# Performance work log

Measured on AMD Instinct MI355X. Metric: run time of the kernel, lower is better.

Reference implementation:

```python
import jax, jax.numpy as jnp
import numpy as np

N_NODES = 10000
N_EDGES = 320000
IN_FEATS = 500
CONV_DIMS = [500, 256, 256]
FC_DIMS = [256, 128, 40]
BN_EPS = 1e-5


def setup_inputs() -> dict:
    key = jax.random.key(0)
    ks = jax.random.split(key, 16)
    inp = {
        "x": jax.random.normal(ks[0], (N_NODES, IN_FEATS), dtype=jnp.float32),
        "edge_index": jax.random.randint(ks[1], (2, N_EDGES), 0, N_NODES, dtype=jnp.int64),
    }
    # conv layer params: Linear W [in,out], b [out]; BatchNorm gamma/beta [out]
    ki = 2
    for li in range(len(CONV_DIMS) - 1):
        d_in, d_out = CONV_DIMS[li], CONV_DIMS[li + 1]
        s = 1.0 / np.sqrt(d_in)
        inp[f"conv_W{li}"] = jax.random.uniform(ks[ki], (d_in, d_out), jnp.float32, -s, s); ki += 1
        inp[f"conv_b{li}"] = jax.random.uniform(ks[ki], (d_out,), jnp.float32, -s, s); ki += 1
        inp[f"bn_g{li}"] = jnp.ones((d_out,), jnp.float32)
        inp[f"bn_b{li}"] = jnp.zeros((d_out,), jnp.float32)
    for li in range(len(FC_DIMS) - 1):
        d_in, d_out = FC_DIMS[li], FC_DIMS[li + 1]
        s = 1.0 / np.sqrt(d_in)
        inp[f"fc_W{li}"] = jax.random.uniform(ks[ki], (d_in, d_out), jnp.float32, -s, s); ki += 1
        inp[f"fc_b{li}"] = jax.random.uniform(ks[ki], (d_out,), jnp.float32, -s, s); ki += 1
    return inp


def _degree(edge_index, n, dtype):
    # Faithful to: A = eye(N); A[i,j] = 1 per edge (set semantics dedupes repeats).
    A = jnp.eye(n, dtype=dtype).at[edge_index[0], edge_index[1]].set(1.0)
    return A.sum(axis=1)  # deg_i = rowsum of A


def _batchnorm(h, g, b):
    # training-mode BatchNorm1d: batch stats, biased variance
    mean = h.mean(axis=0)
    var = h.var(axis=0)
    return (h - mean) * jax.lax.rsqrt(var + BN_EPS) * g + b


def reference(x, edge_index, conv_W0, conv_b0, bn_g0, bn_b0,
              conv_W1, conv_b1, bn_g1, bn_b1,
              fc_W0, fc_b0, fc_W1, fc_b1):
    n = x.shape[0]
    deg = _degree(edge_index, n, x.dtype)
    # D = sqrt(diag(deg)) is a diagonal matrix, so elementwise D*A*D = diag(deg);
    # mm(D*A*D, x) == deg[:, None] * x (exactly the original math).
    h = x
    for W, b, g, beta in ((conv_W0, conv_b0, bn_g0, bn_b0),
                          (conv_W1, conv_b1, bn_g1, bn_b1)):
        h = (deg[:, None] * h) @ W + b
        h = jax.nn.relu(h)
        h = _batchnorm(h, g, beta)
        # dropout: identity at inference
    for W, b in ((fc_W0, fc_b0), (fc_W1, fc_b1)):
        h = jax.nn.relu(h @ W + b)  # original appends ReLU after every fc, incl. last
    return h
```

## Files before the change

kernel.cpp:

```cpp
#include <hip/hip_runtime.h>

#define NN 10000
#define NE 320000
#define MP 10112
#define BN_EPS 1e-5f

#define NRANGE 64
#define BROWS 160
#define NBUCK 128
#define HBITS 5120
#define HWORDS 160
#define SUBCAP 128
#define EPB   5000

typedef __attribute__((ext_vector_type(8))) short short8;
typedef __attribute__((ext_vector_type(4))) float f32x4;
typedef unsigned short u16;

__device__ __forceinline__ void split1(float v, u16& h, u16& l) {
    unsigned int u = __float_as_uint(v);
    h = (u16)(u >> 16);
    float hf = __uint_as_float(u & 0xFFFF0000u);
    l = (u16)(__float_as_uint(v - hf) >> 16);
}

__device__ __forceinline__ void gll16(const void* g, void* l) {
    __builtin_amdgcn_global_load_lds(
        (const __attribute__((address_space(1))) unsigned int*)g,
        (__attribute__((address_space(3))) unsigned int*)l, 16, 0, 0);
}

__device__ void splitW_dev(const float* __restrict__ W, int K, int N, int Kp, int Np,
                           u16* __restrict__ Wt, int bx, int by, char* smem) {
    float (*tile)[65] = (float(*)[65])smem;
    int t = threadIdx.x;
    int bk = bx * 64, bn = by * 64;
    #pragma unroll
    for (int p = 0; p < 4; ++p) {
        int kk = (t >> 4) + p * 16;
        int nc = (t & 15) * 4;
        int k = bk + kk;
        float4 v = {0.f, 0.f, 0.f, 0.f};
        if (k < K && bn + nc + 3 < N)
            v = *(const float4*)&W[(size_t)k * N + bn + nc];
        tile[kk][nc] = v.x; tile[kk][nc + 1] = v.y;
        tile[kk][nc + 2] = v.z; tile[kk][nc + 3] = v.w;
    }
    __syncthreads();
    int nn = t >> 2;
    int kk0 = (t & 3) * 16;
    u16 hs[16], ls[16];
    #pragma unroll
    for (int j = 0; j < 16; ++j) split1(tile[kk0 + j][nn], hs[j], ls[j]);
    size_t ob = (size_t)(bn + nn) * Kp + bk + kk0;
    size_t lo = (size_t)Np * Kp;
    *(short8*)&Wt[ob] = *(short8*)hs;
    *(short8*)&Wt[ob + 8] = *(short8*)&hs[8];
    *(short8*)&Wt[lo + ob] = *(short8*)ls;
    *(short8*)&Wt[lo + ob + 8] = *(short8*)&ls[8];
}

__global__ __launch_bounds__(256)
void scatter_prep(const int* __restrict__ ei,
                  unsigned* __restrict__ bucketArr, unsigned* __restrict__ cnts,
                  float* __restrict__ stats, float* __restrict__ zpad,
                  const float* __restrict__ W0, const float* __restrict__ fW1,
                  u16* __restrict__ W0t, u16* __restrict__ fW1t) {
    __shared__ char smem[16704];
    __shared__ unsigned cnt[NBUCK];
    int b = blockIdx.x;
    int t = threadIdx.x;
    if (b < 64) {
        if (t < NBUCK) cnt[t] = 0;
        __syncthreads();
        int base = b * EPB;
        #pragma unroll
        for (int k = 0; k < 20; ++k) {
            int el = t + k * 256;
            if (el < EPB) {
                int e = base + el;
                unsigned i = (unsigned)ei[e], j = (unsigned)ei[NE + e];
                unsigned bk = (i / BROWS) * 2 + (j >= HBITS ? 1u : 0u);
                unsigned key = (i << 14) | j;
                unsigned pos = atomicAdd(&cnt[bk], 1u);
                if (pos < SUBCAP)
                    bucketArr[((size_t)bk << 13) + ((unsigned)b << 7) + pos] = key;
            }
        }
        __syncthreads();
        if (t < NBUCK) cnts[(t << 6) + b] = min(cnt[t], (unsigned)SUBCAP);
    } else if (b < 96) {
        int idx = b - 64;
        splitW_dev(W0, 500, 256, 512, 256, W0t, idx & 7, idx >> 3, smem);
    } else {
        int base = (b - 96) * 512;
        stats[base + t] = 0.f;
        stats[base + 256 + t] = 0.f;
        if (b == 96 && t < 64) zpad[t] = 0.f;
        splitW_dev(fW1, 128, 40, 128, 64, fW1t, b - 96, 0, smem);
    }
}

__global__ __launch_bounds__(256)
void bucket_degree(const unsigned* __restrict__ bucketArr,
                   const unsigned* __restrict__ cnts,
                   float* __restrict__ degh) {
    __shared__ unsigned lbm[BROWS * HWORDS];
    int b = blockIdx.x, t = threadIdx.x;
    int rr = b >> 1, h = b & 1;
    int row0 = rr * BROWS;
    {
        uint4* z = (uint4*)lbm;
        #pragma unroll
        for (int i = 0; i < 25; ++i) z[t + i * 256] = (uint4){0u, 0u, 0u, 0u};
    }
    __syncthreads();
    for (int r = t; r < BROWS; r += 256) {
        int i = row0 + r;
        if (i < NN && ((i >= HBITS) == (h == 1))) {
            int jj = i - h * HBITS;
            atomicOr(&lbm[r * HWORDS + (jj >> 5)], 1u << (jj & 31));
        }
    }
    {
        int sb = t >> 2, kl = t & 3;
        unsigned n = cnts[(b << 6) + sb];
        const unsigned* keys = bucketArr + ((size_t)b << 13) + ((unsigned)sb << 7);
        for (unsigned k = kl; k < n; k += 4) {
            unsigned key = keys[k];
            unsigned i = key >> 14, j = key & 0x3FFFu;
            unsigned r = i - row0;
            unsigned jj = j - h * HBITS;
            atomicOr(&lbm[r * HWORDS + (jj >> 5)], 1u << (jj & 31));
        }
    }
    __syncthreads();
    #pragma unroll
    for (int pass = 0; pass < 3; ++pass) {
        int r = pass * 64 + (t >> 2), wl = t & 3;
        if (r >= BROWS) break;
        int i = row0 + r;
        int c = 0;
        const uint4* rp = (const uint4*)&lbm[r * HWORDS + wl * 40];
        #pragma unroll
        for (int m = 0; m < 10; ++m) {
            uint4 v = rp[m];
            c += __popc(v.x) + __popc(v.y) + __popc(v.z) + __popc(v.w);
        }
        c += __shfl_down(c, 1, 4);
        c += __shfl_down(c, 2, 4);
        if (wl == 0 && i < MP) degh[h * MP + i] = (float)c;
    }
}

__global__ __launch_bounds__(256, 3)
void conv0_gemm(const float* __restrict__ x, const float* __restrict__ zpad,
                const u16* __restrict__ Bhi, const u16* __restrict__ Blo,
                const float* __restrict__ degh, const float* __restrict__ bias,
                float* __restrict__ stats,
                u16* __restrict__ Ohi, u16* __restrict__ Olo) {
    __shared__ char smem[49152];
    __shared__ float sdeg[64];
    const int Kp = 512, M = NN, No = 256;
    const int b = blockIdx.x;
    const int xcd = b & 7, g = b >> 3;
    const int bx = g & 3, by = (g >> 2) * 8 + xcd;
    if (by >= 158) return;
    const int t = threadIdx.x;
    const int lane = t & 63;
    const int w = t >> 6;
    const int q = lane >> 4;
    const int l16 = lane & 15;
    const int m7 = l16 & 7;
    const int row0 = by * 64;
    const int col0 = bx * 64;

    const u16* srcs[4];
    unsigned dstoff[4];
    #pragma unroll
    for (int i = 0; i < 4; ++i) {
        int j = w + (i & 1) * 4;
        int plane = i >> 1;
        int r = j * 8 + (lane >> 3);
        int c = (lane & 7) ^ (r & 7);
        srcs[i] = (plane ? Blo : Bhi) + (size_t)(col0 + r) * Kp + c * 8;
        dstoff[i] = 16384 + plane * 8192 + j * 1024;
    }

    int xrow[4];
    int xcol[4];
    unsigned xdst[4];
    #pragma unroll
    for (int i = 0; i < 4; ++i) {
        int slab = w * 4 + i;
        int row = slab * 4 + (lane >> 4);
        int cl = (lane & 15) ^ (row & 15);
        xrow[i] = row0 + row;
        xcol[i] = cl * 4;
        xdst[i] = 32768 + slab * 1024;
    }

    #pragma unroll
    for (int i = 0; i < 4; ++i) gll16(srcs[i], smem + dstoff[i]);
    #pragma unroll
    for (int i = 0; i < 4; ++i) {
        int col = xcol[i];
        const float* s = (xrow[i] < NN && col < 500)
                       ? x + (size_t)xrow[i] * 500 + col : zpad;
        gll16(s, smem + xdst[i]);
    }

    if (t < 64) sdeg[t] = degh[row0 + t] + degh[MP + row0 + t];

    __syncthreads();

    const int rn = t & 63;
    const int c4 = t >> 6;
// ... 66 lines not shown
            if (k0 + 128 < Kp) {
                #pragma unroll
                for (int i = 0; i < 4; ++i) {
                    int col = k0 + 128 + xcol[i];
                    const float* s = (xrow[i] < NN && col < 500)
                                   ? x + (size_t)xrow[i] * 500 + col : zpad;
                    gll16(s, smem + xdst[i]);
                }
            }
        }
        #pragma unroll
        for (int kc = 0; kc < 2; ++kc)
            #pragma unroll
            for (int s = 0; s < 4; ++s) {
                acc[s] = __builtin_amdgcn_mfma_f32_16x16x32_bf16(al[kc], bh[kc][s], acc[s], 0, 0, 0);
                acc[s] = __builtin_amdgcn_mfma_f32_16x16x32_bf16(ah[kc], bl[kc][s], acc[s], 0, 0, 0);
                acc[s] = __builtin_amdgcn_mfma_f32_16x16x32_bf16(ah[kc], bh[kc][s], acc[s], 0, 0, 0);
            }
    }

    int growb = row0 + w * 16 + q * 4;
    float dgv[4];
    #pragma unroll
    for (int r = 0; r < 4; ++r) {
        int grow = growb + r;
        dgv[r] = (grow < M) ? sdeg[grow - row0] : 0.f;
    }
    #pragma unroll
    for (int s = 0; s < 4; ++s) {
        int gc = col0 + s * 16 + l16;
        float bia = bias[gc];
        float s_sum = 0.f, ss_sum = 0.f;
        #pragma unroll
        for (int r = 0; r < 4; ++r) {
            int grow = growb + r;
            bool real = grow < M;
            float v = fmaxf(fmaf(dgv[r], acc[s][r], bia), 0.f);
            if (!real) v = 0.f;
            s_sum += v; ss_sum += v * v;
            float vo = v * dgv[r];
            u16 h, l; split1(vo, h, l);
            Ohi[(size_t)grow * No + gc] = h;
            Olo[(size_t)grow * No + gc] = l;
        }
        s_sum  += __shfl_xor(s_sum, 16);  s_sum  += __shfl_xor(s_sum, 32);
        ss_sum += __shfl_xor(ss_sum, 16); ss_sum += __shfl_xor(ss_sum, 32);
        if (lane < 16) {
            atomicAdd(&stats[gc], s_sum);
            atomicAdd(&stats[256 + gc], ss_sum);
        }
    }
}

__global__ __launch_bounds__(256, 4)
void conv1_fold(const u16* __restrict__ Ahi, const u16* __restrict__ Alo,
                const float* __restrict__ W1, const float* __restrict__ stats0,
                const float* __restrict__ g0, const float* __restrict__ bb0,
                const float* __restrict__ b1, const float* __restrict__ degh,
                float* __restrict__ stats1, u16* __restrict__ Ohi, u16* __restrict__ Olo) {
    __shared__ char smem[32768];
    __shared__ float scl[256], sh[256], cred[256], cvec[64];
    const int Kp = 256, M = NN, No = 256;
    const int b = blockIdx.x;
    const int xcd = b & 7, g = b >> 3;
    const int bx = g & 3, by = (g >> 2) * 8 + xcd;
    if (by >= 158) return;
    const int t = threadIdx.x;
    const int lane = t & 63;
    const int w = t >> 6;
    const int q = lane >> 4;
    const int l16 = lane & 15;
    const int m7 = l16 & 7;
    const int row0 = by * 64;
    const int col0 = bx * 64;

    const u16* srcs[4];
    unsigned dstoff[4];
    #pragma unroll
    for (int i = 0; i < 4; ++i) {
        int gi = w + i * 4;
        int plane = gi >> 3, j = gi & 7;
        int r = j * 8 + (lane >> 3);
        int c = (lane & 7) ^ (r & 7);
        srcs[i] = (plane ? Alo : Ahi) + (size_t)(row0 + r) * Kp + c * 8;
        dstoff[i] = plane * 8192 + j * 1024;
    }
    #pragma unroll
    for (int i = 0; i < 4; ++i) { gll16(srcs[i], smem + dstoff[i]); srcs[i] += 64; }

    {
        float mean = stats0[t] * (1.f / NN);
        float var = stats0[256 + t] * (1.f / NN) - mean * mean;
        float s = g0[t] * rsqrtf(var + BN_EPS);
        scl[t] = s;
        sh[t] = bb0[t] - mean * s;
    }
    __syncthreads();
    {
        float s = 0.f;
        int n = col0 + (t & 63);
        #pragma unroll 8
        for (int k = (t >> 6); k < 256; k += 4)
            s += sh[k] * W1[(size_t)k * 256 + n];
        cred[t] = s;
        __syncthreads();
        if (t < 64) cvec[t] = cred[t] + cred[t + 64] + cred[t + 128] + cred[t + 192];
    }
    const int bn = t & 63;
    const int kb = (t >> 6) * 16;
    const int ch0 = (t >> 6) * 2;
    float vals[16];
    {
        const float* wp = W1 + (size_t)kb * 256 + col0 + bn;
        #pragma unroll
        for (int i = 0; i < 16; ++i) vals[i] = wp[(size_t)i * 256] * scl[kb + i];
    }
// ... 29 lines not shown
            }
        }
        __syncthreads();
        if (k0 + 64 < Kp) {
            #pragma unroll
            for (int i = 0; i < 4; ++i) { gll16(srcs[i], smem + dstoff[i]); srcs[i] += 64; }
            const float* wp = W1 + (size_t)(k0 + 64 + kb) * 256 + col0 + bn;
            #pragma unroll
            for (int i = 0; i < 16; ++i) vals[i] = wp[(size_t)i * 256] * scl[k0 + 64 + kb + i];
        }
        #pragma unroll
        for (int kc = 0; kc < 2; ++kc)
            #pragma unroll
            for (int s = 0; s < 4; ++s) {
                acc[s] = __builtin_amdgcn_mfma_f32_16x16x32_bf16(al[kc], bh[kc][s], acc[s], 0, 0, 0);
                acc[s] = __builtin_amdgcn_mfma_f32_16x16x32_bf16(ah[kc], bl[kc][s], acc[s], 0, 0, 0);
                acc[s] = __builtin_amdgcn_mfma_f32_16x16x32_bf16(ah[kc], bh[kc][s], acc[s], 0, 0, 0);
            }
    }

    int growb = row0 + w * 16 + q * 4;
    float dgv[4];
    #pragma unroll
    for (int r = 0; r < 4; ++r) {
        int grow = growb + r;
        dgv[r] = (grow < M) ? (degh[grow] + degh[MP + grow]) : 0.f;
    }
    #pragma unroll
    for (int s = 0; s < 4; ++s) {
        int gc = col0 + s * 16 + l16;
        float bia = b1[gc];
        float cv = cvec[s * 16 + l16];
        float s_sum = 0.f, ss_sum = 0.f;
        #pragma unroll
        for (int r = 0; r < 4; ++r) {
            int grow = growb + r;
            bool real = grow < M;
            float v = fmaxf(fmaf(dgv[r], cv, acc[s][r] + bia), 0.f);
            if (!real) v = 0.f;
            s_sum += v; ss_sum += v * v;
            u16 h, l; split1(v, h, l);
            Ohi[(size_t)grow * No + gc] = h;
            Olo[(size_t)grow * No + gc] = l;
        }
        s_sum  += __shfl_xor(s_sum, 16);  s_sum  += __shfl_xor(s_sum, 32);
        ss_sum += __shfl_xor(ss_sum, 16); ss_sum += __shfl_xor(ss_sum, 32);
        if (lane < 16) {
            atomicAdd(&stats1[gc], s_sum);
            atomicAdd(&stats1[256 + gc], ss_sum);
        }
    }
}

__global__ __launch_bounds__(256, 4)
void fc0_fold(const u16* __restrict__ Ahi, const u16* __restrict__ Alo,
              const float* __restrict__ fW0, const float* __restrict__ stats1,
              const float* __restrict__ g1, const float* __restrict__ bb1,
              const float* __restrict__ fb0,
              u16* __restrict__ Ohi, u16* __restrict__ Olo) {
    __shared__ char smem[32768];
    __shared__ float scl[256], sh[256], cred[256], biasf[64];
    const int Kp = 256, M = NN, No = 128;
    const int b = blockIdx.x;
    const int xcd = b & 7, g = b >> 3;
    const int bx = g & 1, by = (g >> 1) * 8 + xcd;
    if (by >= 158) return;
    const int t = threadIdx.x;
    const int lane = t & 63;
    const int w = t >> 6;
    const int q = lane >> 4;
    const int l16 = lane & 15;
    const int m7 = l16 & 7;
    const int row0 = by * 64;
    const int col0 = bx * 64;

    const u16* srcs[4];
    unsigned dstoff[4];
    #pragma unroll
    for (int i = 0; i < 4; ++i) {
        int gi = w + i * 4;
        int plane = gi >> 3, j = gi & 7;
        int r = j * 8 + (lane >> 3);
        int c = (lane & 7) ^ (r & 7);
        srcs[i] = (plane ? Alo : Ahi) + (size_t)(row0 + r) * Kp + c * 8;
        dstoff[i] = plane * 8192 + j * 1024;
    }
    #pragma unroll
    for (int i = 0; i < 4; ++i) { gll16(srcs[i], smem + dstoff[i]); srcs[i] += 64; }

    {
        float mean = stats1[t] * (1.f / NN);
        float var = stats1[256 + t] * (1.f / NN) - mean * mean;
        float s = g1[t] * rsqrtf(var + BN_EPS);
        scl[t] = s;
        sh[t] = bb1[t] - mean * s;
    }
    __syncthreads();
    {
        float s = 0.f;
        int n = col0 + (t & 63);
        #pragma unroll 8
        for (int k = (t >> 6); k < 256; k += 4)
            s += sh[k] * fW0[(size_t)k * 128 + n];
        cred[t] = s;
        __syncthreads();
        if (t < 64)
            biasf[t] = fb0[col0 + t] + cred[t] + cred[t + 64] + cred[t + 128] + cred[t + 192];
    }
    const int bn = t & 63;
    const int kb = (t >> 6) * 16;
    const int ch0 = (t >> 6) * 2;
    float vals[16];
    {
        const float* wp = fW0 + (size_t)kb * 128 + col0 + bn;
        #pragma unroll
        for (int i = 0; i < 16; ++i) vals[i] = wp[(size_t)i * 128] * scl[kb + i];
    }

    f32x4 acc[4];
    #pragma unroll
    for (int s = 0; s < 4; ++s) acc[s] = (f32x4){0.f, 0.f, 0.f, 0.f};

    for (int k0 = 0; k0 < Kp; k0 += 64) {
        {
            u16 hs[16], ls[16];
            #pragma unroll
            for (int i = 0; i < 16; ++i) split1(vals[i], hs[i], ls[i]);
            unsigned o0 = bn * 128 + ((ch0 ^ (bn & 7)) * 16);
            unsigned o1 = bn * 128 + (((ch0 + 1) ^ (bn & 7)) * 16);
            *(short8*)(smem + 16384 + o0) = *(short8*)&hs[0];
            *(short8*)(smem + 16384 + o1) = *(short8*)&hs[8];
            *(short8*)(smem + 24576 + o0) = *(short8*)&ls[0];
            *(short8*)(smem + 24576 + o1) = *(short8*)&ls[8];
        }
        __syncthreads();
        short8 ah[2], al[2], bh[2][4], bl[2][4];
        #pragma unroll
        for (int kc = 0; kc < 2; ++kc) {
            int aoff = (w * 16 + l16) * 128 + (((kc * 4 + q) ^ m7) * 16);
            ah[kc] = *(const short8*)(smem + aoff);
            al[kc] = *(const short8*)(smem + 8192 + aoff);
            #pragma unroll
            for (int s = 0; s < 4; ++s) {
                int boff = (s * 16 + l16) * 128 + (((kc * 4 + q) ^ m7) * 16);
                bh[kc][s] = *(const short8*)(smem + 16384 + boff);
                bl[kc][s] = *(const short8*)(smem + 24576 + boff);
            }
        }
        __syncthreads();
        if (k0 + 64 < Kp) {
            #pragma unroll
            for (int i = 0; i < 4; ++i) { gll16(srcs[i], smem + dstoff[i]); srcs[i] += 64; }
            const float* wp = fW0 + (size_t)(k0 + 64 + kb) * 128 + col0 + bn;
            #pragma unroll
            for (int i = 0; i < 16; ++i) vals[i] = wp[(size_t)i * 128] * scl[k0 + 64 + kb + i];
        }
        #pragma unroll
        for (int kc = 0; kc < 2; ++kc)
            #pragma unroll
            for (int s = 0; s < 4; ++s) {
                acc[s] = __builtin_amdgcn_mfma_f32_16x16x32_bf16(al[kc], bh[kc][s], acc[s], 0, 0, 0);
                acc[s] = __builtin_amdgcn_mfma_f32_16x16x32_bf16(ah[kc], bl[kc][s], acc[s], 0, 0, 0);
                acc[s] = __builtin_amdgcn_mfma_f32_16x16x32_bf16(ah[kc], bh[kc][s], acc[s], 0, 0, 0);
            }
    }

    int growb = row0 + w * 16 + q * 4;
    #pragma unroll
    for (int s = 0; s < 4; ++s) {
        int gc = col0 + s * 16 + l16;
        float bia = biasf[s * 16 + l16];
        #pragma unroll
        for (int r = 0; r < 4; ++r) {
            int grow = growb + r;
            float v = fmaxf(acc[s][r] + bia, 0.f);
            if (grow >= M) v = 0.f;
            u16 h, l; split1(v, h, l);
            Ohi[(size_t)grow * No + gc] = h;
            Olo[(size_t)grow * No + gc] = l;
        }
    }
}

__global__ __launch_bounds__(256, 3)
void fc1_gemm(const u16* __restrict__ Ahi, const u16* __restrict__ Alo,
              const u16* __restrict__ Bhi, const u16* __restrict__ Blo,
              const float* __restrict__ bias, float* __restrict__ out) {
    __shared__ char smem[32768];
    const int Kp = 128, M = NN, N = 40, No = 40;
    const int t = threadIdx.x;
    const int lane = t & 63;
    const int w = t >> 6;
    const int q = lane >> 4;
    const int l16 = lane & 15;
    const int m7 = l16 & 7;
    const int row0 = blockIdx.x * 64;
    const int col0 = 0;

    const u16* bases[4] = {Ahi, Alo, Bhi, Blo};
    const u16* srcs[8];
    unsigned dstoff[8];
    #pragma unroll
    for (int i = 0; i < 8; ++i) {
        int gi = w + i * 4;
        int reg = i >> 1;
        int j = gi & 7;
        int rb = (reg < 2) ? row0 : col0;
        int r = j * 8 + (lane >> 3);
        int c = (lane & 7) ^ (r & 7);
        srcs[i] = bases[reg] + (size_t)(rb + r) * Kp + c * 8;
        dstoff[i] = reg * 8192 + j * 1024;
    }

    f32x4 acc[4];
    #pragma unroll
    for (int s = 0; s < 4; ++s) acc[s] = (f32x4){0.f, 0.f, 0.f, 0.f};

    #pragma unroll
    for (int i = 0; i < 8; ++i) { gll16(srcs[i], smem + dstoff[i]); srcs[i] += 64; }

    for (int k0 = 0; k0 < Kp; k0 += 64) {
        __syncthreads();
        short8 ah[2], al[2], bh[2][4], bl[2][4];
        #pragma unroll
        for (int kc = 0; kc < 2; ++kc) {
            int aoff = (w * 16 + l16) * 128 + (((kc * 4 + q) ^ m7) * 16);
            ah[kc] = *(const short8*)(smem + aoff);
            al[kc] = *(const short8*)(smem + 8192 + aoff);
            #pragma unroll
            for (int s = 0; s < 4; ++s) {
                int boff = (s * 16 + l16) * 128 + (((kc * 4 + q) ^ m7) * 16);
                bh[kc][s] = *(const short8*)(smem + 16384 + boff);
                bl[kc][s] = *(const short8*)(smem + 24576 + boff);
            }
        }
        __syncthreads();
        if (k0 + 64 < Kp) {
            #pragma unroll
            for (int i = 0; i < 8; ++i) { gll16(srcs[i], smem + dstoff[i]); srcs[i] += 64; }
        }
        #pragma unroll
        for (int kc = 0; kc < 2; ++kc)
            #pragma unroll
            for (int s = 0; s < 4; ++s) {
                acc[s] = __builtin_amdgcn_mfma_f32_16x16x32_bf16(al[kc], bh[kc][s], acc[s], 0, 0, 0);
                acc[s] = __builtin_amdgcn_mfma_f32_16x16x32_bf16(ah[kc], bl[kc][s], acc[s], 0, 0, 0);
                acc[s] = __builtin_amdgcn_mfma_f32_16x16x32_bf16(ah[kc], bh[kc][s], acc[s], 0, 0, 0);
            }
    }

    int growb = row0 + w * 16 + q * 4;
    #pragma unroll
    for (int s = 0; s < 4; ++s) {
        int gc = col0 + s * 16 + l16;
        if (gc >= N) continue;
        float bia = bias[gc];
        #pragma unroll
        for (int r = 0; r < 4; ++r) {
            int grow = growb + r;
            if (grow < M)
                out[(size_t)grow * No + gc] = fmaxf(acc[s][r] + bia, 0.f);
        }
    }
}


extern "C" void kernel_launch(void* const* d_in, const int* in_sizes, int n_in,
                              void* d_out, int out_size, void* d_ws, size_t ws_size,
                              hipStream_t stream) {
    const float* x   = (const float*)d_in[0];
    const int*   ei  = (const int*)d_in[1];
    const float* W0  = (const float*)d_in[2];
    const float* b0  = (const float*)d_in[3];
    const float* g0  = (const float*)d_in[4];
    const float* bb0 = (const float*)d_in[5];
    const float* W1  = (const float*)d_in[6];
    const float* b1  = (const float*)d_in[7];
    const float* g1  = (const float*)d_in[8];
    const float* bb1 = (const float*)d_in[9];
    const float* fW0 = (const float*)d_in[10];
    const float* fb0 = (const float*)d_in[11];
    const float* fW1 = (const float*)d_in[12];
    const float* fb1 = (const float*)d_in[13];
    float* out = (float*)d_out;

    char* ws = (char*)d_ws;
    auto carve = [&](size_t bytes) { char* q = ws; ws += (bytes + 255) & ~(size_t)255; return q; };

    float* stats = (float*)carve(4096);
    float* zpad  = (float*)carve(1024);
    unsigned* cnts = (unsigned*)carve((size_t)NBUCK * 64 * 4);
    float* degh = (float*)carve((size_t)2 * MP * 4);
    unsigned* bucketArr = (unsigned*)carve((size_t)NBUCK * 64 * SUBCAP * 4);
    u16* W0t    = (u16*)carve((size_t)2 * 256 * 512 * 2);
    u16* fW1t   = (u16*)carve((size_t)2 * 64 * 128 * 2);
    u16* H1     = (u16*)carve((size_t)2 * MP * 256 * 2);
    u16* H2     = (u16*)carve((size_t)2 * MP * 256 * 2);
    u16* H3     = (u16*)carve((size_t)2 * MP * 128 * 2);

    dim3 blk(256);

    scatter_prep<<<98, blk, 0, stream>>>(ei, bucketArr, cnts, stats, zpad, W0, fW1, W0t, fW1t);
    bucket_degree<<<NBUCK, blk, 0, stream>>>(bucketArr, cnts, degh);
    conv0_gemm<<<640, blk, 0, stream>>>(
        x, zpad, W0t, W0t + 256 * 512, degh, b0, stats, H1, H1 + (size_t)MP * 256);
    conv1_fold<<<640, blk, 0, stream>>>(
        H1, H1 + (size_t)MP * 256, W1, stats, g0, bb0, b1, degh,
        stats + 512, H2, H2 + (size_t)MP * 256);
    fc0_fold<<<320, blk, 0, stream>>>(
        H2, H2 + (size_t)MP * 256, fW0, stats + 512, g1, bb1, fb0,
        H3, H3 + (size_t)MP * 128);
    fc1_gemm<<<158, blk, 0, stream>>>(
        H3, H3 + (size_t)MP * 128, fW1t, fW1t + 64 * 128, fb1, out);
}
```

Baseline: 177.7 us.

## Fuse four GEMM stages into one cooperative kernel with grid syncs

Turns the conv0, conv1, fc0 and fc1 kernels into device functions and runs them in sequence inside a single cooperative kernel of 640 blocks, with grid.sync between stages. The aim is to remove three kernel launch boundaries and their tail and drain costs. In exchange, every stage now runs under the 3-blocks-per-CU launch bound and shared-memory footprint of the largest stage, and each stage boundary pays for a grid-wide barrier. If the cooperative launch fails, it falls back to the original four separate launches.

```diff
diff --git a/kernel.cpp b/kernel.cpp
--- a/kernel.cpp
+++ b/kernel.cpp
@@ -1,4 +1,5 @@
 #include <hip/hip_runtime.h>
+#include <hip/hip_cooperative_groups.h>
 
 #define NN 10000
 #define NE 320000
@@ -153,16 +154,15 @@
     }
 }
 
-__global__ __launch_bounds__(256, 3)
-void conv0_gemm(const float* __restrict__ x, const float* __restrict__ zpad,
+
+__device__ __forceinline__
+void conv0_body(int b, const float* __restrict__ x, const float* __restrict__ zpad,
                 const u16* __restrict__ Bhi, const u16* __restrict__ Blo,
                 const float* __restrict__ degh, const float* __restrict__ bias,
                 float* __restrict__ stats,
-                u16* __restrict__ Ohi, u16* __restrict__ Olo) {
-    __shared__ char smem[49152];
-    __shared__ float sdeg[64];
+                u16* __restrict__ Ohi, u16* __restrict__ Olo,
+                char* smem, float* sdeg) {
     const int Kp = 512, M = NN, No = 256;
-    const int b = blockIdx.x;
     const int xcd = b & 7, g = b >> 3;
     const int bx = g & 3, by = (g >> 2) * 8 + xcd;
     if (by >= 158) return;
@@ -335,16 +335,18 @@
     }
 }
 
-__global__ __launch_bounds__(256, 4)
-void conv1_fold(const u16* __restrict__ Ahi, const u16* __restrict__ Alo,
+__device__ __forceinline__
+void conv1_body(int b, const u16* __restrict__ Ahi, const u16* __restrict__ Alo,
                 const float* __restrict__ W1, const float* __restrict__ stats0,
                 const float* __restrict__ g0, const float* __restrict__ bb0,
                 const float* __restrict__ b1, const float* __restrict__ degh,
-                float* __restrict__ stats1, u16* __restrict__ Ohi, u16* __restrict__ Olo) {
-    __shared__ char smem[32768];
-    __shared__ float scl[256], sh[256], cred[256], cvec[64];
+                float* __restrict__ stats1, u16* __restrict__ Ohi, u16* __restrict__ Olo,
+                char* smem, float* saux) {
+    float* scl = saux;
+    float* sh = saux + 256;
+    float* cred = saux + 512;
+    float* cvec = saux + 768;
     const int Kp = 256, M = NN, No = 256;
-    const int b = blockIdx.x;
     const int xcd = b & 7, g = b >> 3;
     const int bx = g & 3, by = (g >> 2) * 8 + xcd;
     if (by >= 158) return;
@@ -480,16 +482,18 @@
     }
 }
 
-__global__ __launch_bounds__(256, 4)
-void fc0_fold(const u16* __restrict__ Ahi, const u16* __restrict__ Alo,
+__device__ __forceinline__
+void fc0_body(int b, const u16* __restrict__ Ahi, const u16* __restrict__ Alo,
               const float* __restrict__ fW0, const float* __restrict__ stats1,
               const float* __restrict__ g1, const float* __restrict__ bb1,
               const float* __restrict__ fb0,
-              u16* __restrict__ Ohi, u16* __restrict__ Olo) {
-    __shared__ char smem[32768];
-    __shared__ float scl[256], sh[256], cred[256], biasf[64];
+              u16* __restrict__ Ohi, u16* __restrict__ Olo,
+              char* smem, float* saux) {
+    float* scl = saux;
+    float* sh = saux + 256;
+    float* cred = saux + 512;
+    float* biasf = saux + 768;
     const int Kp = 256, M = NN, No = 128;
-    const int b = blockIdx.x;
     const int xcd = b & 7, g = b >> 3;
     const int bx = g & 1, by = (g >> 1) * 8 + xcd;
     if (by >= 158) return;
@@ -610,11 +614,10 @@
     }
 }
 
-__global__ __launch_bounds__(256, 3)
-void fc1_gemm(const u16* __restrict__ Ahi, const u16* __restrict__ Alo,
+__device__ __forceinline__
+void fc1_body(int b, const u16* __restrict__ Ahi, const u16* __restrict__ Alo,
               const u16* __restrict__ Bhi, const u16* __restrict__ Blo,
-              const float* __restrict__ bias, float* __restrict__ out) {
-    __shared__ char smem[32768];
+              const float* __restrict__ bias, float* __restrict__ out, char* smem) {
     const int Kp = 128, M = NN, N = 40, No = 40;
     const int t = threadIdx.x;
     const int lane = t & 63;
@@ -622,7 +625,7 @@
     const int q = lane >> 4;
     const int l16 = lane & 15;
     const int m7 = l16 & 7;
-    const int row0 = blockIdx.x * 64;
+    const int row0 = b * 64;
     const int col0 = 0;
 
     const u16* bases[4] = {Ahi, Alo, Bhi, Blo};
@@ -690,6 +693,72 @@
                 out[(size_t)grow * No + gc] = fmaxf(acc[s][r] + bia, 0.f);
         }
     }
+}
+
+
+__global__ __launch_bounds__(256, 3)
+void conv0_gemm(const float* __restrict__ x, const float* __restrict__ zpad,
+                const u16* __restrict__ Bhi, const u16* __restrict__ Blo,
+                const float* __restrict__ degh, const float* __restrict__ bias,
+                float* __restrict__ stats,
+                u16* __restrict__ Ohi, u16* __restrict__ Olo) {
+    __shared__ char smem[49152];
+    __shared__ float saux[64];
+    conv0_body(blockIdx.x, x, zpad, Bhi, Blo, degh, bias, stats, Ohi, Olo, smem, saux);
+}
+
+__global__ __launch_bounds__(256, 4)
+void conv1_fold(const u16* __restrict__ Ahi, const u16* __restrict__ Alo,
+                const float* __restrict__ W1, const float* __restrict__ stats0,
+                const float* __restrict__ g0, const float* __restrict__ bb0,
+                const float* __restrict__ b1, const float* __restrict__ degh,
+                float* __restrict__ stats1, u16* __restrict__ Ohi, u16* __restrict__ Olo) {
+    __shared__ char smem[32768];
+    __shared__ float saux[832];
+    conv1_body(blockIdx.x, Ahi, Alo, W1, stats0, g0, bb0, b1, degh, stats1, Ohi, Olo, smem, saux);
+}
+
+__global__ __launch_bounds__(256, 4)
+void fc0_fold(const u16* __restrict__ Ahi, const u16* __restrict__ Alo,
+              const float* __restrict__ fW0, const float* __restrict__ stats1,
+              const float* __restrict__ g1, const float* __restrict__ bb1,
+              const float* __restrict__ fb0,
+              u16* __restrict__ Ohi, u16* __restrict__ Olo) {
+    __shared__ char smem[32768];
+    __shared__ float saux[832];
+    fc0_body(blockIdx.x, Ahi, Alo, fW0, stats1, g1, bb1, fb0, Ohi, Olo, smem, saux);
+}
+
+__global__ __launch_bounds__(256, 3)
+void fc1_gemm(const u16* __restrict__ Ahi, const u16* __restrict__ Alo,
+              const u16* __restrict__ Bhi, const u16* __restrict__ Blo,
+              const float* __restrict__ bias, float* __restrict__ out) {
+    __shared__ char smem[32768];
+    fc1_body(blockIdx.x, Ahi, Alo, Bhi, Blo, bias, out, smem);
+}
+
+__global__ __launch_bounds__(256, 3)
+void mega_gemm(const float* x, const float* zpad, const u16* Bhi, const u16* Blo,
+               const float* degh, const float* b0, float* stats, u16* H1hi, u16* H1lo,
+               const float* W1, const float* g0, const float* bb0, const float* b1,
+               float* stats1, u16* H2hi, u16* H2lo,
+               const float* fW0, const float* g1, const float* bb1, const float* fb0,
+               u16* H3hi, u16* H3lo,
+               const u16* fBhi, const u16* fBlo, const float* fb1, float* out) {
+    __shared__ char smem[49152];
+    __shared__ float saux[832];
+    cooperative_groups::grid_group grid = cooperative_groups::this_grid();
+    const int b = blockIdx.x;
+
+    conv0_body(b, x, zpad, Bhi, Blo, degh, b0, stats, H1hi, H1lo, smem, saux);
+    grid.sync();
+    conv1_body(b, H1hi, H1lo, W1, stats, g0, bb0, b1, degh, stats1, H2hi, H2lo, smem, saux);
+    grid.sync();
+    if (b < 320)
+        fc0_body(b, H2hi, H2lo, fW0, stats1, g1, bb1, fb0, H3hi, H3lo, smem, saux);
+    grid.sync();
+    if (b < 158)
+        fc1_body(b, H3hi, H3lo, fBhi, fBlo, fb1, out, smem);
 }
 
 
@@ -730,14 +799,38 @@
 
     scatter_prep<<<98, blk, 0, stream>>>(ei, bucketArr, cnts, stats, zpad, W0, fW1, W0t, fW1t);
     bucket_degree<<<NBUCK, blk, 0, stream>>>(bucketArr, cnts, degh);
-    conv0_gemm<<<640, blk, 0, stream>>>(
-        x, zpad, W0t, W0t + 256 * 512, degh, b0, stats, H1, H1 + (size_t)MP * 256);
-    conv1_fold<<<640, blk, 0, stream>>>(
-        H1, H1 + (size_t)MP * 256, W1, stats, g0, bb0, b1, degh,
-        stats + 512, H2, H2 + (size_t)MP * 256);
-    fc0_fold<<<320, blk, 0, stream>>>(
-        H2, H2 + (size_t)MP * 256, fW0, stats + 512, g1, bb1, fb0,
-        H3, H3 + (size_t)MP * 128);
-    fc1_gemm<<<158, blk, 0, stream>>>(
-        H3, H3 + (size_t)MP * 128, fW1t, fW1t + 64 * 128, fb1, out);
-}
+
+    {
+        const u16* Bhi = W0t;
+        const u16* Blo = W0t + 256 * 512;
+        u16* H1hi = H1; u16* H1lo = H1 + (size_t)MP * 256;
+        u16* H2hi = H2; u16* H2lo = H2 + (size_t)MP * 256;
+        u16* H3hi = H3; u16* H3lo = H3 + (size_t)MP * 128;
+        const u16* fBhi = fW1t;
+        const u16* fBlo = fW1t + 64 * 128;
+        float* stats1 = stats + 512;
+
+        void* args[] = {
+            (void*)&x, (void*)&zpad, (void*)&Bhi, (void*)&Blo, (void*)&degh,
+            (void*)&b0, (void*)&stats, (void*)&H1hi, (void*)&H1lo,
+            (void*)&W1, (void*)&g0, (void*)&bb0, (void*)&b1, (void*)&stats1,
+            (void*)&H2hi, (void*)&H2lo,
+            (void*)&fW0, (void*)&g1, (void*)&bb1, (void*)&fb0,
+            (void*)&H3hi, (void*)&H3lo,
+            (void*)&fBhi, (void*)&fBlo, (void*)&fb1, (void*)&out};
+
+        hipError_t err = hipLaunchCooperativeKernel(mega_gemm, dim3(640), blk,
+                                                    args, 0u, stream);
+        if (err != hipSuccess) {
+            (void)hipGetLastError();
+            conv0_gemm<<<640, blk, 0, stream>>>(
+                x, zpad, Bhi, Blo, degh, b0, stats, H1hi, H1lo);
+            conv1_fold<<<640, blk, 0, stream>>>(
+                H1hi, H1lo, W1, stats, g0, bb0, b1, degh, stats1, H2hi, H2lo);
+            fc0_fold<<<320, blk, 0, stream>>>(
+                H2hi, H2lo, fW0, stats1, g1, bb1, fb0, H3hi, H3lo);
+            fc1_gemm<<<158, blk, 0, stream>>>(
+                H3hi, H3lo, fBhi, fBlo, fb1, out);
+        }
+    }
+}
```

Result: slower. 435.8 us (+145.3%).

## Fuse fc0 and fc1 GEMMs into one kernel and merge prep into degree kernel

Applied to the files above, without the earlier changes.

Fuses the two fully connected layers so each 64-row block computes the fc0 output for all 128 columns, keeps it in registers and shared memory, and immediately multiplies by the split fc1 weights. This removes the intermediate H3 global buffer and one launch. The weight splitting and stats zeroing move from the edge bucketing kernel into the degree kernel, keeping the kernel count down. The tradeoff is fewer blocks (157) for the FC stage, each doing more serial work, and lower occupancy from the larger shared memory footprint.

```diff
diff --git a/kernel.cpp b/kernel.cpp
--- a/kernel.cpp
+++ b/kernel.cpp
@@ -61,95 +61,95 @@
 }
 
 __global__ __launch_bounds__(256)
-void scatter_prep(const int* __restrict__ ei,
-                  unsigned* __restrict__ bucketArr, unsigned* __restrict__ cnts,
-                  float* __restrict__ stats, float* __restrict__ zpad,
-                  const float* __restrict__ W0, const float* __restrict__ fW1,
-                  u16* __restrict__ W0t, u16* __restrict__ fW1t) {
-    __shared__ char smem[16704];
+void edge_bucketize(const int* __restrict__ ei,
+                    unsigned* __restrict__ bucketArr, unsigned* __restrict__ cnts) {
     __shared__ unsigned cnt[NBUCK];
     int b = blockIdx.x;
     int t = threadIdx.x;
-    if (b < 64) {
-        if (t < NBUCK) cnt[t] = 0;
+    if (t < NBUCK) cnt[t] = 0;
+    __syncthreads();
+    int base = b * EPB;
+    #pragma unroll
+    for (int k = 0; k < 20; ++k) {
+        int el = t + k * 256;
+        if (el < EPB) {
+            int e = base + el;
+            unsigned i = (unsigned)ei[e], j = (unsigned)ei[NE + e];
+            unsigned bk = (i / BROWS) * 2 + (j >= HBITS ? 1u : 0u);
+            unsigned key = (i << 14) | j;
+            unsigned pos = atomicAdd(&cnt[bk], 1u);
+            if (pos < SUBCAP)
+                bucketArr[((size_t)bk << 13) + ((unsigned)b << 7) + pos] = key;
+        }
+    }
+    __syncthreads();
+    if (t < NBUCK) cnts[(t << 6) + b] = min(cnt[t], (unsigned)SUBCAP);
+}
+
+__global__ __launch_bounds__(256)
+void degree_prep(const unsigned* __restrict__ bucketArr,
+                 const unsigned* __restrict__ cnts,
+                 float* __restrict__ degh,
+                 float* __restrict__ stats, float* __restrict__ zpad,
+                 const float* __restrict__ W0, const float* __restrict__ fW1,
+                 u16* __restrict__ W0t, u16* __restrict__ fW1t) {
+    __shared__ char smem[102400];
+    int b = blockIdx.x, t = threadIdx.x;
+    if (b < NBUCK) {
+        unsigned* lbm = (unsigned*)smem;
+        int rr = b >> 1, h = b & 1;
+        int row0 = rr * BROWS;
+        {
+            uint4* z = (uint4*)lbm;
+            #pragma unroll
+            for (int i = 0; i < 25; ++i) z[t + i * 256] = (uint4){0u, 0u, 0u, 0u};
+        }
         __syncthreads();
-        int base = b * EPB;
-        #pragma unroll
-        for (int k = 0; k < 20; ++k) {
-            int el = t + k * 256;
-            if (el < EPB) {
-                int e = base + el;
-                unsigned i = (unsigned)ei[e], j = (unsigned)ei[NE + e];
-                unsigned bk = (i / BROWS) * 2 + (j >= HBITS ? 1u : 0u);
-                unsigned key = (i << 14) | j;
-                unsigned pos = atomicAdd(&cnt[bk], 1u);
-                if (pos < SUBCAP)
-                    bucketArr[((size_t)bk << 13) + ((unsigned)b << 7) + pos] = key;
+        for (int r = t; r < BROWS; r += 256) {
+            int i = row0 + r;
+            if (i < NN && ((i >= HBITS) == (h == 1))) {
+                int jj = i - h * HBITS;
+                atomicOr(&lbm[r * HWORDS + (jj >> 5)], 1u << (jj & 31));
+            }
+        }
+        {
+            int sb = t >> 2, kl = t & 3;
+            unsigned n = cnts[(b << 6) + sb];
+            const unsigned* keys = bucketArr + ((size_t)b << 13) + ((unsigned)sb << 7);
+            for (unsigned k = kl; k < n; k += 4) {
+                unsigned key = keys[k];
+                unsigned i = key >> 14, j = key & 0x3FFFu;
+                unsigned r = i - row0;
+                unsigned jj = j - h * HBITS;
+                atomicOr(&lbm[r * HWORDS + (jj >> 5)], 1u << (jj & 31));
             }
         }
         __syncthreads();
-        if (t < NBUCK) cnts[(t << 6) + b] = min(cnt[t], (unsigned)SUBCAP);
-    } else if (b < 96) {
-        int idx = b - 64;
+        #pragma unroll
+        for (int pass = 0; pass < 3; ++pass) {
+            int r = pass * 64 + (t >> 2), wl = t & 3;
+            if (r >= BROWS) break;
+            int i = row0 + r;
+            int c = 0;
+            const uint4* rp = (const uint4*)&lbm[r * HWORDS + wl * 40];
+            #pragma unroll
+            for (int m = 0; m < 10; ++m) {
+                uint4 v = rp[m];
+                c += __popc(v.x) + __popc(v.y) + __popc(v.z) + __popc(v.w);
+            }
+            c += __shfl_down(c, 1, 4);
+            c += __shfl_down(c, 2, 4);
+            if (wl == 0 && i < MP) degh[h * MP + i] = (float)c;
+        }
+    } else if (b < 160) {
+        int idx = b - 128;
         splitW_dev(W0, 500, 256, 512, 256, W0t, idx & 7, idx >> 3, smem);
     } else {
-        int base = (b - 96) * 512;
+        int base = (b - 160) * 512;
         stats[base + t] = 0.f;
         stats[base + 256 + t] = 0.f;
-        if (b == 96 && t < 64) zpad[t] = 0.f;
-        splitW_dev(fW1, 128, 40, 128, 64, fW1t, b - 96, 0, smem);
-    }
-}
-
-__global__ __launch_bounds__(256)
-void bucket_degree(const unsigned* __restrict__ bucketArr,
-                   const unsigned* __restrict__ cnts,
-                   float* __restrict__ degh) {
-    __shared__ unsigned lbm[BROWS * HWORDS];
-    int b = blockIdx.x, t = threadIdx.x;
-    int rr = b >> 1, h = b & 1;
-    int row0 = rr * BROWS;
-    {
-        uint4* z = (uint4*)lbm;
-        #pragma unroll
-        for (int i = 0; i < 25; ++i) z[t + i * 256] = (uint4){0u, 0u, 0u, 0u};
-    }
-    __syncthreads();
-    for (int r = t; r < BROWS; r += 256) {
-        int i = row0 + r;
-        if (i < NN && ((i >= HBITS) == (h == 1))) {
-            int jj = i - h * HBITS;
-            atomicOr(&lbm[r * HWORDS + (jj >> 5)], 1u << (jj & 31));
-        }
-    }
-    {
-        int sb = t >> 2, kl = t & 3;
-        unsigned n = cnts[(b << 6) + sb];
-        const unsigned* keys = bucketArr + ((size_t)b << 13) + ((unsigned)sb << 7);
-        for (unsigned k = kl; k < n; k += 4) {
-            unsigned key = keys[k];
-            unsigned i = key >> 14, j = key & 0x3FFFu;
-            unsigned r = i - row0;
-            unsigned jj = j - h * HBITS;
-            atomicOr(&lbm[r * HWORDS + (jj >> 5)], 1u << (jj & 31));
-        }
-    }
-    __syncthreads();
-    #pragma unroll
-    for (int pass = 0; pass < 3; ++pass) {
-        int r = pass * 64 + (t >> 2), wl = t & 3;
-        if (r >= BROWS) break;
-        int i = row0 + r;
-        int c = 0;
-        const uint4* rp = (const uint4*)&lbm[r * HWORDS + wl * 40];
-        #pragma unroll
-        for (int m = 0; m < 10; ++m) {
-            uint4 v = rp[m];
-            c += __popc(v.x) + __popc(v.y) + __popc(v.z) + __popc(v.w);
-        }
-        c += __shfl_down(c, 1, 4);
-        c += __shfl_down(c, 2, 4);
-        if (wl == 0 && i < MP) degh[h * MP + i] = (float)c;
+        if (b == 160 && t < 64) zpad[t] = 0.f;
+        splitW_dev(fW1, 128, 40, 128, 64, fW1t, b - 160, 0, smem);
     }
 }
 
@@ -480,19 +480,17 @@
     }
 }
 
-__global__ __launch_bounds__(256, 4)
-void fc0_fold(const u16* __restrict__ Ahi, const u16* __restrict__ Alo,
+__global__ __launch_bounds__(256, 3)
+void fc_fused(const u16* __restrict__ Ahi, const u16* __restrict__ Alo,
               const float* __restrict__ fW0, const float* __restrict__ stats1,
               const float* __restrict__ g1, const float* __restrict__ bb1,
               const float* __restrict__ fb0,
-              u16* __restrict__ Ohi, u16* __restrict__ Olo) {
-    __shared__ char smem[32768];
-    __shared__ float scl[256], sh[256], cred[256], biasf[64];
-    const int Kp = 256, M = NN, No = 128;
-    const int b = blockIdx.x;
-    const int xcd = b & 7, g = b >> 3;
-    const int bx = g & 1, by = (g >> 1) * 8 + xcd;
-    if (by >= 158) return;
+              const u16* __restrict__ Whi, const u16* __restrict__ Wlo,
+              const float* __restrict__ fb1, float* __restrict__ out) {
+    __shared__ char smem[49152];
+    __shared__ float scl[256], sh[256], cred[256], biasf[128];
+    const int M = NN;
+    const int by = blockIdx.x;
     const int t = threadIdx.x;
     const int lane = t & 63;
     const int w = t >> 6;
@@ -500,21 +498,20 @@
     const int l16 = lane & 15;
     const int m7 = l16 & 7;
     const int row0 = by * 64;
-    const int col0 = bx * 64;
-
-    const u16* srcs[4];
-    unsigned dstoff[4];
+
+    const u16* asrc[4];
+    unsigned adst[4];
     #pragma unroll
     for (int i = 0; i < 4; ++i) {
         int gi = w + i * 4;
         int plane = gi >> 3, j = gi & 7;
         int r = j * 8 + (lane >> 3);
         int c = (lane & 7) ^ (r & 7);
-        srcs[i] = (plane ? Alo : Ahi) + (size_t)(row0 + r) * Kp + c * 8;
-        dstoff[i] = plane * 8192 + j * 1024;
-    }
-    #pragma unroll
-    for (int i = 0; i < 4; ++i) { gll16(srcs[i], smem + dstoff[i]); srcs[i] += 64; }
+        asrc[i] = (plane ? Alo : Ahi) + (size_t)(row0 + r) * 256 + c * 8;
+        adst[i] = plane * 8192 + j * 1024;
+    }
+    #pragma unroll
+    for (int i = 0; i < 4; ++i) gll16(asrc[i], smem + adst[i]);
 
     {
         float mean = stats1[t] * (1.f / NN);
@@ -525,63 +522,158 @@
     }
     __syncthreads();
     {
+        int col = t & 127, half = t >> 7;
         float s = 0.f;
-        int n = col0 + (t & 63);
         #pragma unroll 8
-        for (int k = (t >> 6); k < 256; k += 4)
-            s += sh[k] * fW0[(size_t)k * 128 + n];
+        for (int k = half * 128; k < half * 128 + 128; ++k)
+            s += sh[k] * fW0[(size_t)k * 128 + col];
         cred[t] = s;
-        __syncthreads();
-        if (t < 64)
-            biasf[t] = fb0[col0 + t] + cred[t] + cred[t + 64] + cred[t + 128] + cred[t + 192];
-    }
+    }
+    __syncthreads();
+    if (t < 128) biasf[t] = fb0[t] + cred[t] + cred[128 + t];
+
     const int bn = t & 63;
     const int kb = (t >> 6) * 16;
     const int ch0 = (t >> 6) * 2;
-    float vals[16];
+
+    unsigned h3p[2][16];
+    f32x4 acc[4];
+
+    #pragma unroll
+    for (int sub = 0; sub < 2; ++sub) {
+        if (sub) {
+            #pragma unroll
+            for (int i = 0; i < 4; ++i) { asrc[i] -= 192; gll16(asrc[i], smem + adst[i]); }
+        }
+        float vals[16];
+        {
+            const float* wp = fW0 + (size_t)kb * 128 + sub * 64 + bn;
+            #pragma unroll
+            for (int i = 0; i < 16; ++i) vals[i] = wp[(size_t)i * 128] * scl[kb + i];
+        }
+        #pragma unroll
+        for (int s = 0; s < 4; ++s) acc[s] = (f32x4){0.f, 0.f, 0.f, 0.f};
+
+        for (int k0 = 0; k0 < 256; k0 += 64) {
+            {
+                u16 hs[16], ls[16];
+                #pragma unroll
+                for (int i = 0; i < 16; ++i) split1(vals[i], hs[i], ls[i]);
+                unsigned o0 = bn * 128 + ((ch0 ^ (bn & 7)) * 16);
+                unsigned o1 = bn * 128 + (((ch0 + 1) ^ (bn & 7)) * 16);
+                *(short8*)(smem + 16384 + o0) = *(short8*)&hs[0];
+                *(short8*)(smem + 16384 + o1) = *(short8*)&hs[8];
+                *(short8*)(smem + 24576 + o0) = *(short8*)&ls[0];
+                *(short8*)(smem + 24576 + o1) = *(short8*)&ls[8];
+            }
+            __syncthreads();
+            short8 ah[2], al[2], bh[2][4], bl[2][4];
+            #pragma unroll
+            for (int kc = 0; kc < 2; ++kc) {
+                int aoff = (w * 16 + l16) * 128 + (((kc * 4 + q) ^ m7) * 16);
+                ah[kc] = *(const short8*)(smem + aoff);
+                al[kc] = *(const short8*)(smem + 8192 + aoff);
+                #pragma unroll
+                for (int s = 0; s < 4; ++s) {
+                    int boff = (s * 16 + l16) * 128 + (((kc * 4 + q) ^ m7) * 16);
+                    bh[kc][s] = *(const short8*)(smem + 16384 + boff);
+                    bl[kc][s] = *(const short8*)(smem + 24576 + boff);
+                }
+            }
+            __syncthreads();
+            if (k0 + 64 < 256) {
+                #pragma unroll
+                for (int i = 0; i < 4; ++i) { asrc[i] += 64; gll16(asrc[i], smem + adst[i]); }
+                const float* wp = fW0 + (size_t)(k0 + 64 + kb) * 128 + sub * 64 + bn;
+                #pragma unroll
+                for (int i = 0; i < 16; ++i) vals[i] = wp[(size_t)i * 128] * scl[k0 + 64 + kb + i];
+            }
+            #pragma unroll
+            for (int kc = 0; kc < 2; ++kc)
+                #pragma unroll
+                for (int s = 0; s < 4; ++s) {
+                    acc[s] = __builtin_amdgcn_mfma_f32_16x16x32_bf16(al[kc], bh[kc][s], acc[s], 0, 0, 0);
+                    acc[s] = __builtin_amdgcn_mfma_f32_16x16x32_bf16(ah[kc], bl[kc][s], acc[s], 0, 0, 0);
+                    acc[s] = __builtin_amdgcn_mfma_f32_16x16x32_bf16(ah[kc], bh[kc][s], acc[s], 0, 0, 0);
+                }
+        }
+
+        {
+            int growb = row0 + w * 16 + q * 4;
+            #pragma unroll
+            for (int s = 0; s < 4; ++s) {
+                float bia = biasf[sub * 64 + s * 16 + l16];
+                #pragma unroll
+                for (int r = 0; r < 4; ++r) {
+                    float v = fmaxf(acc[s][r] + bia, 0.f);
+                    if (growb + r >= M) v = 0.f;
+                    u16 h, l; split1(v, h, l);
+                    h3p[sub][s * 4 + r] = ((unsigned)h << 16) | l;
+                }
+            }
+        }
+    }
+
+    #pragma unroll
+    for (int i = 0; i < 4; ++i) {
+        int gi = w + i * 4;
+        int plane = gi >> 3, j = gi & 7;
+        int r = j * 8 + (lane >> 3);
+        int c = (lane & 7) ^ (r & 7);
+        const u16* s = (plane ? Wlo : Whi) + (size_t)r * 128 + c * 8;
+        gll16(s, smem + 32768 + plane * 8192 + j * 1024);
+    }
+
     {
-        const float* wp = fW0 + (size_t)kb * 128 + col0 + bn;
-        #pragma unroll
-        for (int i = 0; i < 16; ++i) vals[i] = wp[(size_t)i * 128] * scl[kb + i];
-    }
-
-    f32x4 acc[4];
+        int rl0 = w * 16 + q * 4;
+        #pragma unroll
+        for (int sub = 0; sub < 2; ++sub)
+            #pragma unroll
+            for (int s = 0; s < 4; ++s)
+                #pragma unroll
+                for (int r = 0; r < 4; ++r) {
+                    int rl = rl0 + r;
+                    int kk = s * 16 + l16;
+                    int j = kk >> 3;
+                    unsigned off = (unsigned)sub * 8192 + rl * 128 +
+                                   ((j ^ (rl & 7)) * 16) + (kk & 7) * 2;
+                    unsigned pv = h3p[sub][s * 4 + r];
+                    *(u16*)(smem + off) = (u16)(pv >> 16);
+                    *(u16*)(smem + 16384 + off) = (u16)pv;
+                }
+    }
+
     #pragma unroll
     for (int s = 0; s < 4; ++s) acc[s] = (f32x4){0.f, 0.f, 0.f, 0.f};
 
-    for (int k0 = 0; k0 < Kp; k0 += 64) {
-        {
-            u16 hs[16], ls[16];
-            #pragma unroll
-            for (int i = 0; i < 16; ++i) split1(vals[i], hs[i], ls[i]);
-            unsigned o0 = bn * 128 + ((ch0 ^ (bn & 7)) * 16);
-            unsigned o1 = bn * 128 + (((ch0 + 1) ^ (bn & 7)) * 16);
-            *(short8*)(smem + 16384 + o0) = *(short8*)&hs[0];
-            *(short8*)(smem + 16384 + o1) = *(short8*)&hs[8];
-            *(short8*)(smem + 24576 + o0) = *(short8*)&ls[0];
-            *(short8*)(smem + 24576 + o1) = *(short8*)&ls[8];
+    __syncthreads();
+
+    #pragma unroll
+    for (int st = 0; st < 2; ++st) {
+        short8 ah[2], al[2], bh[2][4], bl[2][4];
+        #pragma unroll
+        for (int kc = 0; kc < 2; ++kc) {
+            int aoff = st * 8192 + (w * 16 + l16) * 128 + (((kc * 4 + q) ^ m7) * 16);
+            ah[kc] = *(const short8*)(smem + aoff);
+            al[kc] = *(const short8*)(smem + 16384 + aoff);
+            #pragma unroll
+            for (int s = 0; s < 4; ++s) {
+                int boff = 32768 + (s * 16 + l16) * 128 + (((kc * 4 + q) ^ m7) * 16);
+                bh[kc][s] = *(const short8*)(smem + boff);
+                bl[kc][s] = *(const short8*)(smem + 8192 + boff);
+            }
         }
         __syncthreads();
-        short8 ah[2], al[2], bh[2][4], bl[2][4];
-        #pragma unroll
-        for (int kc = 0; kc < 2; ++kc) {
-            int aoff = (w * 16 + l16) * 128 + (((kc * 4 + q) ^ m7) * 16);
-            ah[kc] = *(const short8*)(smem + aoff);
-            al[kc] = *(const short8*)(smem + 8192 + aoff);
-            #pragma unroll
-            for (int s = 0; s < 4; ++s) {
-                int boff = (s * 16 + l16) * 128 + (((kc * 4 + q) ^ m7) * 16);
-                bh[kc][s] = *(const short8*)(smem + 16384 + boff);
-                bl[kc][s] = *(const short8*)(smem + 24576 + boff);
-            }
-        }
-        __syncthreads();
-        if (k0 + 64 < Kp) {
-            #pragma unroll
-            for (int i = 0; i < 4; ++i) { gll16(srcs[i], smem + dstoff[i]); srcs[i] += 64; }
-            const float* wp = fW0 + (size_t)(k0 + 64 + kb) * 128 + col0 + bn;
-            #pragma unroll
-            for (int i = 0; i < 16; ++i) vals[i] = wp[(size_t)i * 128] * scl[k0 + 64 + kb + i];
+        if (st == 0) {
+            #pragma unroll
+            for (int i = 0; i < 4; ++i) {
+                int gi = w + i * 4;
+                int plane = gi >> 3, j = gi & 7;
+                int r = j * 8 + (lane >> 3);
+                int c = (lane & 7) ^ (r & 7);
+                const u16* s = (plane ? Wlo : Whi) + (size_t)r * 128 + 64 + c * 8;
+                gll16(s, smem + 32768 + plane * 8192 + j * 1024);
+            }
         }
         #pragma unroll
         for (int kc = 0; kc < 2; ++kc)
@@ -591,103 +683,22 @@
                 acc[s] = __builtin_amdgcn_mfma_f32_16x16x32_bf16(ah[kc], bl[kc][s], acc[s], 0, 0, 0);
                 acc[s] = __builtin_amdgcn_mfma_f32_16x16x32_bf16(ah[kc], bh[kc][s], acc[s], 0, 0, 0);
             }
-    }
-
-    int growb = row0 + w * 16 + q * 4;
-    #pragma unroll
-    for (int s = 0; s < 4; ++s) {
-        int gc = col0 + s * 16 + l16;
-        float bia = biasf[s * 16 + l16];
-        #pragma unroll
-        for (int r = 0; r < 4; ++r) {
-            int grow = growb + r;
-            float v = fmaxf(acc[s][r] + bia, 0.f);
-            if (grow >= M) v = 0.f;
-            u16 h, l; split1(v, h, l);
-            Ohi[(size_t)grow * No + gc] = h;
-            Olo[(size_t)grow * No + gc] = l;
-        }
-    }
-}
-
-__global__ __launch_bounds__(256, 3)
-void fc1_gemm(const u16* __restrict__ Ahi, const u16* __restrict__ Alo,
-              const u16* __restrict__ Bhi, const u16* __restrict__ Blo,
-              const float* __restrict__ bias, float* __restrict__ out) {
-    __shared__ char smem[32768];
-    const int Kp = 128, M = NN, N = 40, No = 40;
-    const int t = threadIdx.x;
-    const int lane = t & 63;
-    const int w = t >> 6;
-    const int q = lane >> 4;
-    const int l16 = lane & 15;
-    const int m7 = l16 & 7;
-    const int row0 = blockIdx.x * 64;
-    const int col0 = 0;
-
-    const u16* bases[4] = {Ahi, Alo, Bhi, Blo};
-    const u16* srcs[8];
-    unsigned dstoff[8];
-    #pragma unroll
-    for (int i = 0; i < 8; ++i) {
-        int gi = w + i * 4;
-        int reg = i >> 1;
-        int j = gi & 7;
-        int rb = (reg < 2) ? row0 : col0;
-        int r = j * 8 + (lane >> 3);
-        int c = (lane & 7) ^ (r & 7);
-        srcs[i] = bases[reg] + (size_t)(rb + r) * Kp + c * 8;
-        dstoff[i] = reg * 8192 + j * 1024;
-    }
-
-    f32x4 acc[4];
-    #pragma unroll
-    for (int s = 0; s < 4; ++s) acc[s] = (f32x4){0.f, 0.f, 0.f, 0.f};
-
-    #pragma unroll
-    for (int i = 0; i < 8; ++i) { gll16(srcs[i], smem + dstoff[i]); srcs[i] += 64; }
-
-    for (int k0 = 0; k0 < Kp; k0 += 64) {
-        __syncthreads();
-        short8 ah[2], al[2], bh[2][4], bl[2][4];
-        #pragma unroll
-        for (int kc = 0; kc < 2; ++kc) {
-            int aoff = (w * 16 + l16) * 128 + (((kc * 4 + q) ^ m7) * 16);
-            ah[kc] = *(const short8*)(smem + aoff);
-            al[kc] = *(const short8*)(smem + 8192 + aoff);
-            #pragma unroll
-            for (int s = 0; s < 4; ++s) {
-                int boff = (s * 16 + l16) * 128 + (((kc * 4 + q) ^ m7) * 16);
-                bh[kc][s] = *(const short8*)(smem + 16384 + boff);
-                bl[kc][s] = *(const short8*)(smem + 24576 + boff);
-            }
-        }
-        __syncthreads();
-        if (k0 + 64 < Kp) {
-            #pragma unroll
-            for (int i = 0; i < 8; ++i) { gll16(srcs[i], smem + dstoff[i]); srcs[i] += 64; }
-        }
-        #pragma unroll
-        for (int kc = 0; kc < 2; ++kc)
-            #pragma unroll
-            for (int s = 0; s < 4; ++s) {
-                acc[s] = __builtin_amdgcn_mfma_f32_16x16x32_bf16(al[kc], bh[kc][s], acc[s], 0, 0, 0);
-                acc[s] = __builtin_amdgcn_mfma_f32_16x16x32_bf16(ah[kc], bl[kc][s], acc[s], 0, 0, 0);
-                acc[s] = __builtin_amdgcn_mfma_f32_16x16x32_bf16(ah[kc], bh[kc][s], acc[s], 0, 0, 0);
-            }
-    }
-
-    int growb = row0 + w * 16 + q * 4;
-    #pragma unroll
-    for (int s = 0; s < 4; ++s) {
-        int gc = col0 + s * 16 + l16;
-        if (gc >= N) continue;
-        float bia = bias[gc];
-        #pragma unroll
-        for (int r = 0; r < 4; ++r) {
-            int grow = growb + r;
-            if (grow < M)
-                out[(size_t)grow * No + gc] = fmaxf(acc[s][r] + bia, 0.f);
+        if (st == 0) __syncthreads();
+    }
+
+    {
+        int growb = row0 + w * 16 + q * 4;
+        #pragma unroll
+        for (int s = 0; s < 4; ++s) {
+            int gc = s * 16 + l16;
+            if (gc >= 40) continue;
+            float bia = fb1[gc];
+            #pragma unroll
+            for (int r = 0; r < 4; ++r) {
+                int grow = growb + r;
+                if (grow < M)
+                    out[(size_t)grow * 40 + gc] = fmaxf(acc[s][r] + bia, 0.f);
+            }
         }
     }
 }
@@ -724,20 +735,18 @@
     u16* fW1t   = (u16*)carve((size_t)2 * 64 * 128 * 2);
     u16* H1     = (u16*)carve((size_t)2 * MP * 256 * 2);
     u16* H2     = (u16*)carve((size_t)2 * MP * 256 * 2);
-    u16* H3     = (u16*)carve((size_t)2 * MP * 128 * 2);
 
     dim3 blk(256);
 
-    scatter_prep<<<98, blk, 0, stream>>>(ei, bucketArr, cnts, stats, zpad, W0, fW1, W0t, fW1t);
-    bucket_degree<<<NBUCK, blk, 0, stream>>>(bucketArr, cnts, degh);
+    edge_bucketize<<<64, blk, 0, stream>>>(ei, bucketArr, cnts);
+    degree_prep<<<162, blk, 0, stream>>>(bucketArr, cnts, degh, stats, zpad,
+                                         W0, fW1, W0t, fW1t);
     conv0_gemm<<<640, blk, 0, stream>>>(
         x, zpad, W0t, W0t + 256 * 512, degh, b0, stats, H1, H1 + (size_t)MP * 256);
     conv1_fold<<<640, blk, 0, stream>>>(
         H1, H1 + (size_t)MP * 256, W1, stats, g0, bb0, b1, degh,
         stats + 512, H2, H2 + (size_t)MP * 256);
-    fc0_fold<<<320, blk, 0, stream>>>(
+    fc_fused<<<157, blk, 0, stream>>>(
         H2, H2 + (size_t)MP * 256, fW0, stats + 512, g1, bb1, fb0,
-        H3, H3 + (size_t)MP * 128);
-    fc1_gemm<<<158, blk, 0, stream>>>(
-        H3, H3 + (size_t)MP * 128, fW1t, fW1t + 64 * 128, fb1, out);
-}
+        fW1t, fW1t + 64 * 128, fb1, out);
+}
```

Measured after the change: 181.5 us. 1.02x slower.
